# Kernel optimization log

Hardware: AMD Instinct MI355X
Metric: run time of the kernel (lower is better)

Reference implementation:

```python
import jax, jax.numpy as jnp
import numpy as np

MODES = 16   # hard-coded in FNO(..., modes=16, width=32)
WIDTH = 32


def setup_inputs() -> dict:
    key = jax.random.key(0)
    ks = jax.random.split(key, 13)
    B, S, IN, E, OUT, L = 4, 256, 1024, 2048, 1024, 4
    s = 0.02
    return {
        "x": jax.random.normal(ks[0], (B, S, IN), jnp.float32),
        "W_en": jax.random.normal(ks[1], (IN, E), jnp.float32) * s,
        "b_en": jnp.zeros((E,), jnp.float32),
        "fc0_w": jax.random.normal(ks[2], (L, 1, WIDTH), jnp.float32) * s,
        "fc0_b": jnp.zeros((L, WIDTH), jnp.float32),
        "spec_wr": jax.random.normal(ks[3], (L, WIDTH, WIDTH, MODES), jnp.float32) / WIDTH,
        "spec_wi": jax.random.normal(ks[4], (L, WIDTH, WIDTH, MODES), jnp.float32) / WIDTH,
        "pw_w": jax.random.normal(ks[5], (L, WIDTH, WIDTH), jnp.float32) * s,
        "pw_b": jnp.zeros((L, WIDTH), jnp.float32),
        "fc1_w": jax.random.normal(ks[6], (L, WIDTH, 1), jnp.float32) * s,
        "fc1_b": jnp.zeros((L, 1), jnp.float32),
        "W_de": jax.random.normal(ks[7], (E, OUT), jnp.float32) * s,
        "b_de": jnp.zeros((OUT,), jnp.float32),
    }


def _fno_block(u, fc0_w, fc0_b, wr, wi, pw_w, pw_b, fc1_w, fc1_b):
    # u: (T, E, 1) -- 1 channel over spatial axis E
    v = u @ fc0_w + fc0_b                       # (T, E, WIDTH) channel lift
    Vf = jnp.fft.rfft(v, axis=1)                # (T, E//2+1, WIDTH) complex
    Wc = wr + 1j * wi                           # (WIDTH, WIDTH, MODES)
    out_m = jnp.einsum("tmc,cdm->tmd", Vf[:, :MODES, :], Wc)
    Of = jnp.zeros_like(Vf).at[:, :MODES, :].set(out_m)
    v1 = jnp.fft.irfft(Of, n=v.shape[1], axis=1)  # spectral conv branch
    v2 = v @ pw_w + pw_b                          # pointwise 1x1 conv branch
    v = jax.nn.gelu(v1 + v2)
    return v @ fc1_w + fc1_b                      # (T, E, 1) channel project


def reference(x, W_en, b_en, fc0_w, fc0_b, spec_wr, spec_wi, pw_w, pw_b, fc1_w, fc1_b, W_de, b_de):
    h = x @ W_en + b_en                          # (B, S, E)
    B, S, E = h.shape
    u = h.reshape(B * S, E, 1)                   # embed axis = FNO spatial axis, 1 channel
    L = fc0_w.shape[0]
    for i in range(L):                           # small fixed layer count
        u = _fno_block(u, fc0_w[i], fc0_b[i], spec_wr[i], spec_wi[i],
                       pw_w[i], pw_b[i], fc1_w[i], fc1_b[i])
    h = u.reshape(B, S, E)
    return h @ W_de + b_de                       # (B, S, OUT)
```

## Files before the change

### kernel.cpp

```cpp
#include <hip/hip_runtime.h>
#include <math.h>

#ifndef M_PI
#define M_PI 3.14159265358979323846
#endif

#define T_ROWS 1024
#define EDIM   2048
#define IN_DIM 1024
#define OUT_DIM 1024
#define NMODES 16
#define NLAYERS 4

typedef __attribute__((ext_vector_type(8))) short bf16x8;
typedef __attribute__((ext_vector_type(4))) float f32x4;
typedef __attribute__((ext_vector_type(2))) float f32x2;

__device__ __forceinline__ unsigned short f2bf(float f) {
  union { float f; unsigned u; } v; v.f = f;
  unsigned r = v.u + 0x7FFFu + ((v.u >> 16) & 1u);
  return (unsigned short)(r >> 16);
}
__device__ __forceinline__ float bf2f(unsigned short h) {
  union { unsigned u; float f; } v; v.u = ((unsigned)h) << 16;
  return v.f;
}
__device__ __forceinline__ void f2bf_split(float v, unsigned short& h, unsigned short& l) {
  h = f2bf(v);
  l = f2bf(v - bf2f(h));
}

__device__ __forceinline__ void transpose_tile(const float* __restrict__ B,
                                               unsigned short* __restrict__ BT,
                                               int K, int N, int k0, int n0, int tid,
                                               float (*tile)[33])
{
  {
    int r = tid >> 3, c4 = (tid & 7) * 4;
    float4 v = *(const float4*)&B[(size_t)(k0 + r) * N + n0 + c4];
    tile[r][c4 + 0] = v.x; tile[r][c4 + 1] = v.y;
    tile[r][c4 + 2] = v.z; tile[r][c4 + 3] = v.w;
  }
  __syncthreads();
  {
    int n = tid >> 3, kq = (tid & 7) * 4;
    ushort4 o;
    o.x = f2bf(tile[kq + 0][n]); o.y = f2bf(tile[kq + 1][n]);
    o.z = f2bf(tile[kq + 2][n]); o.w = f2bf(tile[kq + 3][n]);
    *(ushort4*)&BT[(size_t)(n0 + n) * K + k0 + kq] = o;
  }
}

__global__ __launch_bounds__(256)
void setup_all(float* __restrict__ ctab, float* __restrict__ stab,
               unsigned short* __restrict__ basFh, unsigned short* __restrict__ basFl,
               const float* __restrict__ fc0w, const float* __restrict__ fc0b,
               const float* __restrict__ wr, const float* __restrict__ wi,
               const float* __restrict__ pww, const float* __restrict__ pwb,
               float* __restrict__ Wmr, float* __restrict__ Wmi,
               float* __restrict__ b0r, float* __restrict__ pw1,
               float* __restrict__ pb1,
               const float* __restrict__ W_en, unsigned short* __restrict__ WenT,
               const float* __restrict__ W_de, unsigned short* __restrict__ WdeT,
               const float* __restrict__ x, unsigned short* __restrict__ x_bf)
{
  __shared__ float tile[32][33];
  const int b = blockIdx.x, tid = threadIdx.x;
  if (b < 8) {
    int i = b * 256 + tid;
    double ang = (2.0 * M_PI / (double)EDIM) * (double)i;
    ctab[i] = (float)cos(ang);
    stab[i] = (float)sin(ang);
  } else if (b < 264) {
    int idx = (b - 8) * 256 + tid;
    int mt = idx >> 9;
    int l  = (idx >> 3) & 63;
    int i  = idx & 7;
    int xx = mt * 16 + (l & 15);
    int j  = (l >> 4) * 8 + i;
    float v;
    if (j < 31) {
      int m = (j < NMODES) ? j : (j - 15);
      int ia = (m * xx) & (EDIM - 1);
      float ang = (float)(2.0 * M_PI / (double)EDIM) * (float)ia;
      v = (j < NMODES) ? cosf(ang) : sinf(ang);
    } else {
      v = 1.0f;
    }
    unsigned short h, lo; f2bf_split(v, h, lo);
    basFh[idx] = h; basFl[idx] = lo;
  } else if (b == 264) {
    if (tid >= NLAYERS * 32) return;
    int l = tid >> 5, d = tid & 31;
    for (int m = 0; m < NMODES; ++m) {
      float sr = 0.f, si = 0.f;
      for (int c = 0; c < 32; ++c) {
        float w0 = fc0w[l * 32 + c];
        size_t base = ((size_t)(l * 32 + c) * 32 + d) * NMODES + m;
        sr += w0 * wr[base];
        si += w0 * wi[base];
      }
      Wmr[(l * NMODES + m) * 32 + d] = sr;
      Wmi[(l * NMODES + m) * 32 + d] = si;
    }
    float sb = 0.f, sp = 0.f, sq = 0.f;
    for (int c = 0; c < 32; ++c) {
      float b0 = fc0b[l * 32 + c];
      float w0 = fc0w[l * 32 + c];
      sb += b0 * wr[((size_t)(l * 32 + c) * 32 + d) * NMODES + 0];
      float pw = pww[(size_t)(l * 32 + c) * 32 + d];
      sp += w0 * pw;
      sq += b0 * pw;
    }
    b0r[l * 32 + d] = (float)EDIM * sb;
    pw1[l * 32 + d] = sp;
    pb1[l * 32 + d] = sq + pwb[l * 32 + d];
  } else if (b < 2313) {
    int tb = b - 265;
    int n0 = (tb & 63) * 32, k0 = (tb >> 6) * 32;
    transpose_tile(W_en, WenT, IN_DIM, EDIM, k0, n0, tid, tile);
  } else if (b < 4361) {
    int tb = b - 2313;
    int n0 = (tb & 31) * 32, k0 = (tb >> 5) * 32;
    transpose_tile(W_de, WdeT, EDIM, OUT_DIM, k0, n0, tid, tile);
  } else {
    size_t i0 = ((size_t)(b - 4361) * 256 + tid) * 8;
    float4 a0 = *(const float4*)&x[i0];
    float4 a1 = *(const float4*)&x[i0 + 4];
    ushort4 o0, o1;
    o0.x = f2bf(a0.x); o0.y = f2bf(a0.y); o0.z = f2bf(a0.z); o0.w = f2bf(a0.w);
    o1.x = f2bf(a1.x); o1.y = f2bf(a1.y); o1.z = f2bf(a1.z); o1.w = f2bf(a1.w);
    *(ushort4*)&x_bf[i0]     = o0;
    *(ushort4*)&x_bf[i0 + 4] = o1;
  }
}

#define BKK 64
__global__ __launch_bounds__(256)
void gemm_mfma(const unsigned short* __restrict__ A, const unsigned short* __restrict__ BT,
               const float* __restrict__ bias, float* __restrict__ C,
               int M, int N, int K)
{
  __shared__ __align__(16) unsigned short Asb[2][64 * BKK];
  __shared__ __align__(16) unsigned short Bsb[2][64 * BKK];
  const int tid = threadIdx.x;
  const int bm = blockIdx.y * 64, bn = blockIdx.x * 64;
  const int lane = tid & 63, wave = tid >> 6;
  const int wr = wave >> 1, wc = wave & 1;

  const int srow = tid >> 2;
  const int skq  = tid & 3;

  f32x4 acc[2][2] = {};

  const unsigned short* aRow = A + (size_t)(bm + srow) * K + skq * 16;
  const unsigned short* bRow = BT + (size_t)(bn + srow) * K + skq * 16;

  int slot0 = (skq * 2 + 0) ^ ((srow >> 1) & 7);
  int slot1 = (skq * 2 + 1) ^ ((srow >> 1) & 7);

  bf16x8 pa0, pa1, pb0, pb1v;
  pa0 = *(const bf16x8*)(aRow + 0);
  pa1 = *(const bf16x8*)(aRow + 8);
  pb0 = *(const bf16x8*)(bRow + 0);
  pb1v = *(const bf16x8*)(bRow + 8);
  *(bf16x8*)&Asb[0][srow * BKK + slot0 * 8] = pa0;
  *(bf16x8*)&Asb[0][srow * BKK + slot1 * 8] = pa1;
  *(bf16x8*)&Bsb[0][srow * BKK + slot0 * 8] = pb0;
  *(bf16x8*)&Bsb[0][srow * BKK + slot1 * 8] = pb1v;

  int cur = 0;
  for (int k0 = 0; k0 < K; k0 += BKK) {
    __syncthreads();
    const bool more = (k0 + BKK) < K;
    if (more) {
      pa0 = *(const bf16x8*)(aRow + k0 + BKK);
      pa1 = *(const bf16x8*)(aRow + k0 + BKK + 8);
      pb0 = *(const bf16x8*)(bRow + k0 + BKK);
      pb1v = *(const bf16x8*)(bRow + k0 + BKK + 8);
    }
    #pragma unroll
    for (int s = 0; s < 2; ++s) {
      int kb = s * 4 + (lane >> 4);
      bf16x8 a[2], b[2];
      #pragma unroll
      for (int i = 0; i < 2; ++i) {
        int ar = wr * 32 + i * 16 + (lane & 15);
        a[i] = *(const bf16x8*)&Asb[cur][ar * BKK + (kb ^ ((ar >> 1) & 7)) * 8];
        int br = wc * 32 + i * 16 + (lane & 15);
        b[i] = *(const bf16x8*)&Bsb[cur][br * BKK + (kb ^ ((br >> 1) & 7)) * 8];
      }
      #pragma unroll
      for (int i = 0; i < 2; ++i)
        #pragma unroll
        for (int j = 0; j < 2; ++j)
          acc[i][j] = __builtin_amdgcn_mfma_f32_16x16x32_bf16(a[i], b[j], acc[i][j], 0, 0, 0);
    }
    if (more) {
      const int nxt = cur ^ 1;
      *(bf16x8*)&Asb[nxt][srow * BKK + slot0 * 8] = pa0;
      *(bf16x8*)&Asb[nxt][srow * BKK + slot1 * 8] = pa1;
      *(bf16x8*)&Bsb[nxt][srow * BKK + slot0 * 8] = pb0;
      *(bf16x8*)&Bsb[nxt][srow * BKK + slot1 * 8] = pb1v;
    }
    cur ^= 1;
  }

  #pragma unroll
  for (int j = 0; j < 2; ++j) {
    int col = bn + wc * 32 + j * 16 + (lane & 15);
    float bz = bias[col];
    #pragma unroll
    for (int i = 0; i < 2; ++i)
      #pragma unroll
      for (int r = 0; r < 4; ++r) {
        int row = bm + wr * 32 + i * 16 + (lane >> 4) * 4 + r;
        C[(size_t)row * N + col] = acc[i][j][r] + bz;
      }
  }
}

__global__ __launch_bounds__(256)
void dft_coef(const float* __restrict__ u,
              const float* __restrict__ ctab, const float* __restrict__ stab,
              const float* __restrict__ Wmr, const float* __restrict__ Wmi,
              const float* __restrict__ b0r, const float* __restrict__ pb1,
              unsigned short* __restrict__ coefFh, unsigned short* __restrict__ coefFl)
{
  const int t = blockIdx.x, tid = threadIdx.x;
  __shared__ float dred[32][264];
  __shared__ float Ush[32];

  float pr[NMODES], pi[NMODES];
  #pragma unroll
  for (int m = 0; m < NMODES; ++m) { pr[m] = 0.f; pi[m] = 0.f; }
  #pragma unroll
  for (int it = 0; it < 4; ++it) {
    const int x = tid + it * 256;
    const float v0 = u[(size_t)t * EDIM + x];
    const float v1 = u[(size_t)t * EDIM + x + 1024];
    const float ve = v0 + v1, vo = v0 - v1;
    const float cx = ctab[x], sx = stab[x];
    float c = 1.f, s = 0.f;
    #pragma unroll
    for (int m = 0; m < NMODES; ++m) {
      const float vsel = (m & 1) ? vo : ve;
      pr[m] += vsel * c;
      pi[m] -= vsel * s;
      float cn = c * cx - s * sx;
      s = s * cx + c * sx;
      c = cn;
    }
  }
  #pragma unroll
  for (int m = 0; m < NMODES; ++m) {
    dred[m][tid]          = pr[m];
    dred[NMODES + m][tid] = pi[m];
  }
  __syncthreads();
  {
    const int ch = tid >> 3, p = tid & 7;
    float4 s4 = make_float4(0.f, 0.f, 0.f, 0.f);
    #pragma unroll
    for (int j = 0; j < 8; ++j) {
      const float4 v = *(const float4*)&dred[ch][j * 32 + p * 4];
      s4.x += v.x; s4.y += v.y; s4.z += v.z; s4.w += v.w;
    }
    float ssum = (s4.x + s4.y) + (s4.z + s4.w);
    ssum += __shfl_down(ssum, 4, 64);
    ssum += __shfl_down(ssum, 2, 64);
    ssum += __shfl_down(ssum, 1, 64);
    if (p == 0) Ush[ch] = ssum;
  }
  __syncthreads();

  if (tid < 128) {
    const float invN = 1.0f / (float)EDIM;
    int n = tid >> 6, l = tid & 63;
    int d = n * 16 + (l & 15);
    union { unsigned short u[8]; bf16x8 v; } ph, pl;
    #pragma unroll
    for (int i = 0; i < 8; ++i) {
      int j = (l >> 4) * 8 + i;
      float v;
      if (j < NMODES) {
        int m = j;
        float ofr = Ush[m] * Wmr[m * 32 + d] - Ush[NMODES + m] * Wmi[m * 32 + d];
        v = (m == 0) ? (ofr + b0r[d]) * invN : 2.0f * ofr * invN;
      } else if (j < 31) {
        int m = j - 15;
        float ofi = Ush[m] * Wmi[m * 32 + d] + Ush[NMODES + m] * Wmr[m * 32 + d];
        v = -2.0f * ofi * invN;
      } else {
        v = pb1[d];
      }
      f2bf_split(v, ph.u[i], pl.u[i]);
    }
    size_t base = ((size_t)t * 2 + n) * 64 + l;
    *(bf16x8*)&coefFh[base * 8] = ph.v;
    *(bf16x8*)&coefFl[base * 8] = pl.v;
  }
}

template<int LAST>
__global__ __launch_bounds__(256, 8)
void recon_mfma(float* __restrict__ u,
                unsigned short* __restrict__ u_bf,
                const unsigned short* __restrict__ basFh,
                const unsigned short* __restrict__ basFl,
                const unsigned short* __restrict__ coefFh,
                const unsigned short* __restrict__ coefFl,
                const float* __restrict__ pw1,
                const float* __restrict__ f1w, const float* __restrict__ f1b)
{
  const int t  = blockIdx.x >> 2;
  const int cq = blockIdx.x & 3;
  const int tid = threadIdx.x, lane = tid & 63, w = tid >> 6;
  const int g = lane >> 4, m15 = lane & 15;

  bf16x8 ch[2], cl[2];
  #pragma unroll
  for (int n = 0; n < 2; ++n) {
    size_t base = (((size_t)t * 2 + n) * 64 + lane) * 8;
    ch[n] = *(const bf16x8*)&coefFh[base];
    cl[n] = *(const bf16x8*)&coefFl[base];
  }

  f32x2 pw2[2][2], fv2[2][2];
  #pragma unroll
  for (int n = 0; n < 2; ++n) {
    float4 pv = *(const float4*)&pw1[n * 16 + g * 4];
    float4 fv = *(const float4*)&f1w[n * 16 + g * 4];
    pw2[n][0] = (f32x2){pv.x, pv.y}; pw2[n][1] = (f32x2){pv.z, pv.w};
    fv2[n][0] = (f32x2){fv.x, fv.y}; fv2[n][1] = (f32x2){fv.z, fv.w};
  }
  const float fb = f1b[0];
  float* __restrict__ urow = u + (size_t)t * EDIM;

  const f32x2 kC1 = {0.1029433f, 0.1029433f};
  const f32x2 kC0 = {2.3022082f, 2.3022082f};
  const f32x2 kOne = {1.0f, 1.0f};

  #pragma unroll
  for (int q = 0; q < 8; ++q) {
    const int mt = cq * 32 + w * 8 + q;
    bf16x8 bh = *(const bf16x8*)&basFh[((size_t)mt * 64 + lane) * 8];
    bf16x8 bl = *(const bf16x8*)&basFl[((size_t)mt * 64 + lane) * 8];
    f32x4 acc[2];
    #pragma unroll
    for (int n = 0; n < 2; ++n) {
      f32x4 a = {};
      a = __builtin_amdgcn_mfma_f32_16x16x32_bf16(cl[n], bh, a, 0, 0, 0);
      a = __builtin_amdgcn_mfma_f32_16x16x32_bf16(ch[n], bl, a, 0, 0, 0);
      a = __builtin_amdgcn_mfma_f32_16x16x32_bf16(ch[n], bh, a, 0, 0, 0);
      acc[n] = a;
    }
    const int x = mt * 16 + m15;
    const float uval = urow[x];
    const f32x2 u2 = {uval, uval};
    f32x2 o2 = {0.f, 0.f};
    #pragma unroll
    for (int n = 0; n < 2; ++n) {
      #pragma unroll
      for (int p = 0; p < 2; ++p) {
        f32x2 av = {acc[n][2 * p], acc[n][2 * p + 1]};
        f32x2 s  = __builtin_elementwise_fma(u2, pw2[n][p], av);
        f32x2 s2 = s * s;
        f32x2 tt = __builtin_elementwise_fma(s2, kC1, kC0);
        f32x2 arg = s * tt;
        f32x2 e;
        e.x = __builtin_amdgcn_exp2f(arg.x);
        e.y = __builtin_amdgcn_exp2f(arg.y);
        f32x2 d = e + kOne;
        f32x2 r;
        r.x = __builtin_amdgcn_rcpf(d.x);
        r.y = __builtin_amdgcn_rcpf(d.y);
        f32x2 tgl = __builtin_elementwise_fma(-s, r, s);
        o2 = __builtin_elementwise_fma(tgl, fv2[n][p], o2);
      }
    }
    float o = o2.x + o2.y;
    o += __shfl_xor(o, 16, 64);
    o += __shfl_xor(o, 32, 64);
    if (lane < 16) {
      if (LAST) u_bf[(size_t)t * EDIM + x] = f2bf(o + fb);
      else      urow[x] = o + fb;
    }
  }
}

extern "C" void kernel_launch(void* const* d_in, const int* in_sizes, int n_in,
                              void* d_out, int out_size, void* d_ws, size_t ws_size,
                              hipStream_t stream)
{
  const float* x    = (const float*)d_in[0];
  const float* W_en = (const float*)d_in[1];
  const float* b_en = (const float*)d_in[2];
  const float* fc0w = (const float*)d_in[3];
  const float* fc0b = (const float*)d_in[4];
  const float* swr  = (const float*)d_in[5];
  const float* swi  = (const float*)d_in[6];
  const float* pww  = (const float*)d_in[7];
  const float* pwb  = (const float*)d_in[8];
  const float* f1w  = (const float*)d_in[9];
  const float* f1b  = (const float*)d_in[10];
  const float* W_de = (const float*)d_in[11];
  const float* b_de = (const float*)d_in[12];
  float* out = (float*)d_out;
  float* ws  = (float*)d_ws;

  float* u    = ws;
  float* ctab = u + (size_t)T_ROWS * EDIM;
  float* stab = ctab + EDIM;
  float* Wmr  = stab + EDIM;
  float* Wmi  = Wmr + NLAYERS * NMODES * 32;
  float* b0r  = Wmi + NLAYERS * NMODES * 32;
  float* pw1  = b0r + NLAYERS * 32;
  float* pb1  = pw1 + NLAYERS * 32;
  unsigned short* basFh  = (unsigned short*)(pb1 + NLAYERS * 32);
  unsigned short* basFl  = basFh + 128 * 64 * 8;
  unsigned short* coefFh = basFl + 128 * 64 * 8;
  unsigned short* coefFl = coefFh + (size_t)T_ROWS * 2 * 64 * 8;
  unsigned short* x_bf   = coefFl + (size_t)T_ROWS * 2 * 64 * 8;
  unsigned short* u_bf   = x_bf + (size_t)T_ROWS * IN_DIM;
  unsigned short* WenT   = u_bf + (size_t)T_ROWS * EDIM;
  unsigned short* WdeT   = WenT + (size_t)EDIM * IN_DIM;

  setup_all<<<4873, 256, 0, stream>>>(ctab, stab, basFh, basFl, fc0w, fc0b,
                                      swr, swi, pww, pwb, Wmr, Wmi, b0r, pw1, pb1,
                                      W_en, WenT, W_de, WdeT, x, x_bf);

  { dim3 g(EDIM / 64, T_ROWS / 64);
    gemm_mfma<<<g, 256, 0, stream>>>(x_bf, WenT, b_en, u, T_ROWS, EDIM, IN_DIM); }

  for (int l = 0; l < NLAYERS; ++l) {
    dft_coef<<<T_ROWS, 256, 0, stream>>>(u, ctab, stab,
        Wmr + l * NMODES * 32, Wmi + l * NMODES * 32, b0r + l * 32, pb1 + l * 32,
        coefFh, coefFl);
    if (l < NLAYERS - 1)
      recon_mfma<0><<<4 * T_ROWS, 256, 0, stream>>>(u, u_bf, basFh, basFl,
          coefFh, coefFl, pw1 + l * 32, f1w + l * 32, f1b + l);
    else
      recon_mfma<1><<<4 * T_ROWS, 256, 0, stream>>>(u, u_bf, basFh, basFl,
          coefFh, coefFl, pw1 + l * 32, f1w + l * 32, f1b + l);
  }

  { dim3 g(OUT_DIM / 64, T_ROWS / 64);
    gemm_mfma<<<g, 256, 0, stream>>>(u_bf, WdeT, b_de, out, T_ROWS, OUT_DIM, EDIM); }
}
```

Baseline: 216.5 us.

## Fuse next layer's truncated DFT into recon kernel epilogue, drop dft_coef launches

Each non-final recon_mfma block now computes partial 16-mode DFT sums of the 512 outputs it just produced and writes them to a ping-pong buffer. The following layer sums the four quarter partials and builds its MFMA coefficient fragments in shared memory, so three dft_coef launches and the reread of u are removed. The cost is extra shared memory, more syncthreads and DFT arithmetic inside the recon kernel, which may lower occupancy. The mode recurrence also gives different rounding than the table-based DFT.

```diff
diff --git a/kernel.cpp b/kernel.cpp
--- a/kernel.cpp
+++ b/kernel.cpp
@@ -302,7 +302,7 @@
   }
 }
 
-template<int LAST>
+template<int FIRST, int LAST>
 __global__ __launch_bounds__(256, 8)
 void recon_mfma(float* __restrict__ u,
                 unsigned short* __restrict__ u_bf,
@@ -310,6 +310,11 @@
                 const unsigned short* __restrict__ basFl,
                 const unsigned short* __restrict__ coefFh,
                 const unsigned short* __restrict__ coefFl,
+                const float* __restrict__ UrIn,
+                float* __restrict__ UrOut,
+                const float* __restrict__ ctab, const float* __restrict__ stab,
+                const float* __restrict__ Wmr, const float* __restrict__ Wmi,
+                const float* __restrict__ b0r, const float* __restrict__ pb1,
                 const float* __restrict__ pw1,
                 const float* __restrict__ f1w, const float* __restrict__ f1b)
 {
@@ -318,12 +323,56 @@
   const int tid = threadIdx.x, lane = tid & 63, w = tid >> 6;
   const int g = lane >> 4, m15 = lane & 15;
 
+  __shared__ union SMU {
+    struct { unsigned short cfh[2][64][8]; unsigned short cfl[2][64][8]; } pro;
+    float dred[16][264];
+  } sm;
+  __shared__ float urows[512];
+  __shared__ float Ush[32];
+
   bf16x8 ch[2], cl[2];
-  #pragma unroll
-  for (int n = 0; n < 2; ++n) {
-    size_t base = (((size_t)t * 2 + n) * 64 + lane) * 8;
-    ch[n] = *(const bf16x8*)&coefFh[base];
-    cl[n] = *(const bf16x8*)&coefFl[base];
+  if (FIRST) {
+    #pragma unroll
+    for (int n = 0; n < 2; ++n) {
+      size_t base = (((size_t)t * 2 + n) * 64 + lane) * 8;
+      ch[n] = *(const bf16x8*)&coefFh[base];
+      cl[n] = *(const bf16x8*)&coefFl[base];
+    }
+  } else {
+    if (tid < 32) {
+      const size_t o = (size_t)t * 32 + tid;
+      const size_t TS = (size_t)T_ROWS * 32;
+      Ush[tid] = (UrIn[o] + UrIn[TS + o]) + (UrIn[2 * TS + o] + UrIn[3 * TS + o]);
+    }
+    __syncthreads();
+    if (tid < 128) {
+      const float invN = 1.0f / (float)EDIM;
+      int n = tid >> 6, ll = tid & 63;
+      int d = n * 16 + (ll & 15);
+      #pragma unroll
+      for (int i = 0; i < 8; ++i) {
+        int j = (ll >> 4) * 8 + i;
+        float v;
+        if (j < NMODES) {
+          int m = j;
+          float ofr = Ush[m] * Wmr[m * 32 + d] - Ush[NMODES + m] * Wmi[m * 32 + d];
+          v = (m == 0) ? (ofr + b0r[d]) * invN : 2.0f * ofr * invN;
+        } else if (j < 31) {
+          int m = j - 15;
+          float ofi = Ush[m] * Wmi[m * 32 + d] + Ush[NMODES + m] * Wmr[m * 32 + d];
+          v = -2.0f * ofi * invN;
+        } else {
+          v = pb1[d];
+        }
+        f2bf_split(v, sm.pro.cfh[n][ll][i], sm.pro.cfl[n][ll][i]);
+      }
+    }
+    __syncthreads();
+    #pragma unroll
+    for (int n = 0; n < 2; ++n) {
+      ch[n] = *(const bf16x8*)&sm.pro.cfh[n][lane][0];
+      cl[n] = *(const bf16x8*)&sm.pro.cfl[n][lane][0];
+    }
   }
 
   f32x2 pw2[2][2], fv2[2][2];
@@ -383,8 +432,71 @@
     o += __shfl_xor(o, 16, 64);
     o += __shfl_xor(o, 32, 64);
     if (lane < 16) {
-      if (LAST) u_bf[(size_t)t * EDIM + x] = f2bf(o + fb);
-      else      urow[x] = o + fb;
+      const float of = o + fb;
+      if (LAST) {
+        u_bf[(size_t)t * EDIM + x] = f2bf(of);
+      } else {
+        urow[x] = of;
+        urows[(w * 8 + q) * 16 + m15] = of;
+      }
+    }
+  }
+
+  if (!LAST) {
+    __syncthreads();
+    float pr[NMODES], pi[NMODES];
+    #pragma unroll
+    for (int m = 0; m < NMODES; ++m) { pr[m] = 0.f; pi[m] = 0.f; }
+    #pragma unroll
+    for (int it = 0; it < 2; ++it) {
+      const int xl = tid + it * 256;
+      const int x = cq * 512 + xl;
+      const float val = urows[xl];
+      const float cx = ctab[x], sx = stab[x];
+      float c = 1.f, s = 0.f;
+      #pragma unroll
+      for (int m = 0; m < NMODES; ++m) {
+        pr[m] += val * c;
+        pi[m] -= val * s;
+        float cn = c * cx - s * sx;
+        s = s * cx + c * sx;
+        c = cn;
+      }
+    }
+    #pragma unroll
+    for (int m = 0; m < NMODES; ++m) sm.dred[m][tid] = pr[m];
+    __syncthreads();
+    if (tid < 128) {
+      const int ch2 = tid >> 3, p = tid & 7;
+      float4 s4 = make_float4(0.f, 0.f, 0.f, 0.f);
+      #pragma unroll
+      for (int j = 0; j < 8; ++j) {
+        const float4 v = *(const float4*)&sm.dred[ch2][j * 32 + p * 4];
+        s4.x += v.x; s4.y += v.y; s4.z += v.z; s4.w += v.w;
+      }
+      float ssum = (s4.x + s4.y) + (s4.z + s4.w);
+      ssum += __shfl_down(ssum, 4, 64);
+      ssum += __shfl_down(ssum, 2, 64);
+      ssum += __shfl_down(ssum, 1, 64);
+      if (p == 0) UrOut[((size_t)cq * T_ROWS + t) * 32 + ch2] = ssum;
+    }
+    __syncthreads();
+    #pragma unroll
+    for (int m = 0; m < NMODES; ++m) sm.dred[m][tid] = pi[m];
+    __syncthreads();
+    if (tid < 128) {
+      const int ch2 = tid >> 3, p = tid & 7;
+      float4 s4 = make_float4(0.f, 0.f, 0.f, 0.f);
+      #pragma unroll
+      for (int j = 0; j < 8; ++j) {
+        const float4 v = *(const float4*)&sm.dred[ch2][j * 32 + p * 4];
+        s4.x += v.x; s4.y += v.y; s4.z += v.z; s4.w += v.w;
+      }
+      float ssum = (s4.x + s4.y) + (s4.z + s4.w);
+      ssum += __shfl_down(ssum, 4, 64);
+      ssum += __shfl_down(ssum, 2, 64);
+      ssum += __shfl_down(ssum, 1, 64);
+      if (p == 0) UrOut[((size_t)cq * T_ROWS + t) * 32 + NMODES + ch2] = ssum;
     }
   }
 }
@@ -417,7 +529,9 @@
   float* b0r  = Wmi + NLAYERS * NMODES * 32;
   float* pw1  = b0r + NLAYERS * 32;
   float* pb1  = pw1 + NLAYERS * 32;
-  unsigned short* basFh  = (unsigned short*)(pb1 + NLAYERS * 32);
+  float* UrA  = pb1 + NLAYERS * 32;
+  float* UrB  = UrA + 4 * (size_t)T_ROWS * 32;
+  unsigned short* basFh  = (unsigned short*)(UrB + 4 * (size_t)T_ROWS * 32);
   unsigned short* basFl  = basFh + 128 * 64 * 8;
   unsigned short* coefFh = basFl + 128 * 64 * 8;
   unsigned short* coefFl = coefFh + (size_t)T_ROWS * 2 * 64 * 8;
@@ -433,17 +547,25 @@
   { dim3 g(EDIM / 64, T_ROWS / 64);
     gemm_mfma<<<g, 256, 0, stream>>>(x_bf, WenT, b_en, u, T_ROWS, EDIM, IN_DIM); }
 
-  for (int l = 0; l < NLAYERS; ++l) {
-    dft_coef<<<T_ROWS, 256, 0, stream>>>(u, ctab, stab,
-        Wmr + l * NMODES * 32, Wmi + l * NMODES * 32, b0r + l * 32, pb1 + l * 32,
-        coefFh, coefFl);
-    if (l < NLAYERS - 1)
-      recon_mfma<0><<<4 * T_ROWS, 256, 0, stream>>>(u, u_bf, basFh, basFl,
-          coefFh, coefFl, pw1 + l * 32, f1w + l * 32, f1b + l);
-    else
-      recon_mfma<1><<<4 * T_ROWS, 256, 0, stream>>>(u, u_bf, basFh, basFl,
-          coefFh, coefFl, pw1 + l * 32, f1w + l * 32, f1b + l);
-  }
+  dft_coef<<<T_ROWS, 256, 0, stream>>>(u, ctab, stab,
+      Wmr, Wmi, b0r, pb1, coefFh, coefFl);
+  recon_mfma<1, 0><<<4 * T_ROWS, 256, 0, stream>>>(u, u_bf, basFh, basFl,
+      coefFh, coefFl, UrA, UrA, ctab, stab,
+      Wmr, Wmi, b0r, pb1, pw1, f1w, f1b);
+
+  recon_mfma<0, 0><<<4 * T_ROWS, 256, 0, stream>>>(u, u_bf, basFh, basFl,
+      coefFh, coefFl, UrA, UrB, ctab, stab,
+      Wmr + 1 * NMODES * 32, Wmi + 1 * NMODES * 32, b0r + 1 * 32, pb1 + 1 * 32,
+      pw1 + 1 * 32, f1w + 1 * 32, f1b + 1);
+  recon_mfma<0, 0><<<4 * T_ROWS, 256, 0, stream>>>(u, u_bf, basFh, basFl,
+      coefFh, coefFl, UrB, UrA, ctab, stab,
+      Wmr + 2 * NMODES * 32, Wmi + 2 * NMODES * 32, b0r + 2 * 32, pb1 + 2 * 32,
+      pw1 + 2 * 32, f1w + 2 * 32, f1b + 2);
+
+  recon_mfma<0, 1><<<4 * T_ROWS, 256, 0, stream>>>(u, u_bf, basFh, basFl,
+      coefFh, coefFl, UrA, UrB, ctab, stab,
+      Wmr + 3 * NMODES * 32, Wmi + 3 * NMODES * 32, b0r + 3 * 32, pb1 + 3 * 32,
+      pw1 + 3 * 32, f1w + 3 * 32, f1b + 3);
 
   { dim3 g(OUT_DIM / 64, T_ROWS / 64);
     gemm_mfma<<<g, 256, 0, stream>>>(u_bf, WdeT, b_de, out, T_ROWS, OUT_DIM, EDIM); }
```

Result: slower. 222.1 us (+2.6%).
